# Performance work log

Hardware: AMD Instinct MI355X
Metric: run time of the kernel (lower is better)

## Reference

```python
import jax, jax.numpy as jnp
import numpy as np

NQ = 4
DIM = 1 << NQ  # 16 statevector amplitudes

def _cnot_perm(c, t):
    idx = np.arange(DIM)
    cbit = (idx >> (NQ - 1 - c)) & 1
    return np.where(cbit == 1, idx ^ (1 << (NQ - 1 - t)), idx)

# BasicEntanglerLayers CNOT ring: (0,1),(1,2),(2,3),(3,0)
CNOT_PERMS = [jnp.asarray(_cnot_perm(q, (q + 1) % NQ)) for q in range(NQ)]
_idx = np.arange(DIM)
SIGNS = jnp.asarray(np.stack([1.0 - 2.0 * ((_idx >> (NQ - 1 - q)) & 1) for q in range(NQ)]).astype(np.float32))  # (NQ, DIM), PauliZ eigenvalues


def _apply_rx(state, theta, q):
    """Apply RX(theta) on wire q. state: (N, DIM) complex64. theta: scalar or (N,)."""
    half = theta * 0.5
    c = jnp.cos(half).astype(jnp.complex64)
    js = (1j * jnp.sin(half)).astype(jnp.complex64)
    if jnp.ndim(theta) == 1:
        c = c[:, None, None]
        js = js[:, None, None]
    d1, d2 = 1 << q, 1 << (NQ - 1 - q)
    st = state.reshape(-1, d1, 2, d2)
    a0, a1 = st[:, :, 0, :], st[:, :, 1, :]
    out = jnp.stack([c * a0 - js * a1, c * a1 - js * a0], axis=2)
    return out.reshape(state.shape)


def circuit(angles, weights):
    """AngleEmbedding(RX) + BasicEntanglerLayers(RX + CNOT ring) + <Z_i>.
    angles: (N, NQ) real. weights: (L, NQ). returns (N, NQ)."""
    N = angles.shape[0]
    state = jnp.zeros((N, DIM), jnp.complex64).at[:, 0].set(1.0)
    for q in range(NQ):  # AngleEmbedding: per-sample RX angles
        state = _apply_rx(state, angles[:, q], q)
    for l in range(weights.shape[0]):  # entangler layers (static count)
        for q in range(NQ):
            state = _apply_rx(state, weights[l, q], q)
        for q in range(NQ):
            state = state[:, CNOT_PERMS[q]]
    probs = jnp.real(state) ** 2 + jnp.imag(state) ** 2
    return probs @ SIGNS.T


def setup_inputs() -> dict:
    key = jax.random.key(0)
    ks = jax.random.split(key, 5)
    B, S = 32, 2048
    TWO_PI = 6.2831853
    return {
        "x": jax.random.normal(ks[0], (B, S, NQ), jnp.float32),
        "weights_Q": jax.random.uniform(ks[1], (1, NQ), jnp.float32) * TWO_PI,
        "weights_K": jax.random.uniform(ks[2], (1, NQ), jnp.float32) * TWO_PI,
        "weights_V": jax.random.uniform(ks[3], (1, NQ), jnp.float32) * TWO_PI,
        "weights_C": jax.random.uniform(ks[4], (1, NQ), jnp.float32) * TWO_PI,
    }


def reference(x, weights_Q, weights_K, weights_V, weights_C):
    B, S, E = x.shape  # E == NQ == 4
    flat = x.reshape(B * S, E)
    Q = circuit(flat, weights_Q).reshape(B, S, E)
    K = circuit(flat, weights_K).reshape(B, S, E)
    V = circuit(flat, weights_V).reshape(B, S, E)
    scores = jnp.einsum('bqe,bke->bqk', Q, K) / (E ** 0.5)
    attn = jax.nn.softmax(scores, axis=-1)
    ctx = jnp.einsum('bqk,bke->bqe', attn, V)
    return circuit(ctx.reshape(B * S, E), weights_C).reshape(B, S, E)
```

## Files before the change

### kernel.cpp

```cpp
#include <hip/hip_runtime.h>

#define DIM 16
#define SEQ 2048
#define CHUNK 256
#define NPAIR (CHUNK / 2)
#define NCHUNK 8
#define RPT 2

typedef float v2f __attribute__((ext_vector_type(2)));
typedef float v4f __attribute__((ext_vector_type(4)));

static __device__ __forceinline__ float fexp2(float x) {
#if __has_builtin(__builtin_amdgcn_exp2f)
    return __builtin_amdgcn_exp2f(x);
#else
    return exp2f(x);
#endif
}


template<int P>
__device__ __forceinline__ void rx_bit(float sr[DIM], float si[DIM], float ch, float sh) {
    constexpr int m = 1 << P;
    #pragma unroll
    for (int i = 0; i < DIM; ++i) {
        if ((i & m) == 0) {
            const int j = i | m;
            float r0 = sr[i], i0 = si[i], r1 = sr[j], i1 = si[j];
            sr[i] = fmaf(ch, r0,  sh * i1);
            si[i] = fmaf(ch, i0, -sh * r1);
            sr[j] = fmaf(ch, r1,  sh * i0);
            si[j] = fmaf(ch, i1, -sh * r0);
        }
    }
}

template<int PC, int PT>
__device__ __forceinline__ void cnot_g(float sr[DIM], float si[DIM]) {
    constexpr int cm = 1 << PC, tm = 1 << PT;
    #pragma unroll
    for (int i = 0; i < DIM; ++i) {
        if ((i & cm) && !(i & tm)) {
            const int j = i | tm;
            float t;
            t = sr[i]; sr[i] = sr[j]; sr[j] = t;
            t = si[i]; si[i] = si[j]; si[j] = t;
        }
    }
}

__device__ __forceinline__ void embed(float sr[DIM], float si[DIM], float4 a) {
    float c0, s0, c1, s1, c2, s2, c3, s3;
    __sincosf(0.5f * a.x, &s0, &c0);
    __sincosf(0.5f * a.y, &s1, &c1);
    __sincosf(0.5f * a.z, &s2, &c2);
    __sincosf(0.5f * a.w, &s3, &c3);
    float A[4] = {c0 * c1, c0 * s1, s0 * c1, s0 * s1};
    float B[4] = {c2 * c3, c2 * s3, s2 * c3, s2 * s3};
    #pragma unroll
    for (int idx = 0; idx < DIM; ++idx) {
        const float p = A[idx >> 2] * B[idx & 3];
        const int m = __builtin_popcount(idx) & 3;
        sr[idx] = (m == 0) ? p : (m == 2) ? -p : 0.f;
        si[idx] = (m == 1) ? -p : (m == 3) ? p : 0.f;
    }
}

__device__ __forceinline__ void layer(float sr[DIM], float si[DIM], float4 w) {
    float ch, sh;
    __sincosf(0.5f * w.x, &sh, &ch); rx_bit<3>(sr, si, ch, sh);
    __sincosf(0.5f * w.y, &sh, &ch); rx_bit<2>(sr, si, ch, sh);
    __sincosf(0.5f * w.z, &sh, &ch); rx_bit<1>(sr, si, ch, sh);
    __sincosf(0.5f * w.w, &sh, &ch); rx_bit<0>(sr, si, ch, sh);
    cnot_g<3,2>(sr, si);
    cnot_g<2,1>(sr, si);
    cnot_g<1,0>(sr, si);
    cnot_g<0,3>(sr, si);
}

__device__ __forceinline__ float4 measure(const float sr[DIM], const float si[DIM]) {
    float e0 = 0.f, e1 = 0.f, e2 = 0.f, e3 = 0.f;
    #pragma unroll
    for (int i = 0; i < DIM; ++i) {
        float p = fmaf(sr[i], sr[i], si[i] * si[i]);
        e0 += (i & 8) ? -p : p;
        e1 += (i & 4) ? -p : p;
        e2 += (i & 2) ? -p : p;
        e3 += (i & 1) ? -p : p;
    }
    return make_float4(e0, e1, e2, e3);
}


__global__ __launch_bounds__(256) void qkv_kernel(
        const float* __restrict__ x,
        const float* __restrict__ wQp, const float* __restrict__ wKp,
        const float* __restrict__ wVp,
        float4* __restrict__ Q, float4* __restrict__ KV) {
    const int i = blockIdx.x * 256 + threadIdx.x;
    const int which = blockIdx.y;
    const float4 xv = ((const float4*)x)[i];
    const float* wp = (which == 0) ? wQp : (which == 1) ? wKp : wVp;
    const float4 w = *(const float4*)wp;

    float sr[DIM], si[DIM];
    embed(sr, si, xv);
    layer(sr, si, w);
    const float4 r = measure(sr, si);

    if (which == 0)      Q[i]          = r;
    else if (which == 1) KV[2 * i]     = r;
    else                 KV[2 * i + 1] = r;
}


__global__ __launch_bounds__(256, 4) void attn_partial(
        const float4* __restrict__ Q, const float4* __restrict__ KV,
        float* __restrict__ pden, float4* __restrict__ pctx, int n) {
    __shared__ float4 kvs[4 * NPAIR];

    const int rg = blockIdx.x;
    const int c  = blockIdx.y;
    const int b  = rg >> 2;

    const float4* KVc = KV + (size_t)b * (2 * SEQ) + c * (2 * CHUNK);
    if (threadIdx.x < NPAIR) {
        const int p = threadIdx.x;
        const float4 K0 = KVc[4 * p + 0];
        const float4 V0 = KVc[4 * p + 1];
        const float4 K1 = KVc[4 * p + 2];
        const float4 V1 = KVc[4 * p + 3];
        kvs[4 * p + 0] = make_float4(K0.x, K1.x, K0.y, K1.y);
        kvs[4 * p + 1] = make_float4(K0.z, K1.z, K0.w, K1.w);
        kvs[4 * p + 2] = make_float4(V0.x, V1.x, V0.y, V1.y);
        kvs[4 * p + 3] = make_float4(V0.z, V1.z, V0.w, V1.w);
    }
    __syncthreads();

    const float SC = 0.72134752044f;
    const int row0 = rg * (256 * RPT) + threadIdx.x;

    v2f qx[RPT], qy[RPT], qz[RPT], qw[RPT];
    #pragma unroll
    for (int j = 0; j < RPT; ++j) {
        const float4 q = Q[row0 + j * 256];
        qx[j] = (v2f){q.x * SC, q.x * SC};
        qy[j] = (v2f){q.y * SC, q.y * SC};
        qz[j] = (v2f){q.z * SC, q.z * SC};
        qw[j] = (v2f){q.w * SC, q.w * SC};
    }

    v2f den[RPT], ax[RPT], ay[RPT], az[RPT], aw[RPT];
    #pragma unroll
    for (int j = 0; j < RPT; ++j) {
        den[j] = (v2f){0.f, 0.f};
        ax[j] = den[j]; ay[j] = den[j]; az[j] = den[j]; aw[j] = den[j];
    }

    const v4f* kvp = (const v4f*)kvs;
    #pragma unroll 4
    for (int p = 0; p < NPAIR; ++p) {
        const v4f kA = kvp[4 * p + 0];
        const v4f kB = kvp[4 * p + 1];
        const v4f vA = kvp[4 * p + 2];
        const v4f vB = kvp[4 * p + 3];
        const v2f kx = kA.xy, ky = kA.zw, kz = kB.xy, kw = kB.zw;
        const v2f vx = vA.xy, vy = vA.zw, vz = vB.xy, vw = vB.zw;
        #pragma unroll
        for (int j = 0; j < RPT; ++j) {
            v2f s = __builtin_elementwise_fma(qy[j], ky, qx[j] * kx);
            s     = __builtin_elementwise_fma(qz[j], kz, s);
            s     = __builtin_elementwise_fma(qw[j], kw, s);
            const v2f e = (v2f){fexp2(s.x), fexp2(s.y)};
            den[j] += e;
            ax[j] = __builtin_elementwise_fma(e, vx, ax[j]);
            ay[j] = __builtin_elementwise_fma(e, vy, ay[j]);
            az[j] = __builtin_elementwise_fma(e, vz, az[j]);
            aw[j] = __builtin_elementwise_fma(e, vw, aw[j]);
        }
    }

    #pragma unroll
    for (int j = 0; j < RPT; ++j) {
        const int row = row0 + j * 256;
        pden[c * n + row] = den[j].x + den[j].y;
        pctx[c * n + row] = make_float4(ax[j].x + ax[j].y, ay[j].x + ay[j].y,
                                        az[j].x + az[j].y, aw[j].x + aw[j].y);
    }
}


__global__ __launch_bounds__(256) void combine_kernel(
        const float* __restrict__ pden, const float4* __restrict__ pctx,
        const float* __restrict__ wCp, float4* __restrict__ out, int n) {
    const int row = blockIdx.x * 256 + threadIdx.x;

    float d = 0.f;
    float c0 = 0.f, c1 = 0.f, c2 = 0.f, c3 = 0.f;
    #pragma unroll
    for (int c = 0; c < NCHUNK; ++c) {
        d += pden[c * n + row];
        const float4 p = pctx[c * n + row];
        c0 += p.x; c1 += p.y; c2 += p.z; c3 += p.w;
    }
    const float inv = 1.0f / d;
    const float4 ctx = make_float4(c0 * inv, c1 * inv, c2 * inv, c3 * inv);

    const float4 wC = *(const float4*)wCp;
    float sr[DIM], si[DIM];
    embed(sr, si, ctx);
    layer(sr, si, wC);
    out[row] = measure(sr, si);
}


extern "C" void kernel_launch(void* const* d_in, const int* in_sizes, int n_in,
                              void* d_out, int out_size, void* d_ws, size_t ws_size,
                              hipStream_t stream) {
    const float* x  = (const float*)d_in[0];
    const float* wQ = (const float*)d_in[1];
    const float* wK = (const float*)d_in[2];
    const float* wV = (const float*)d_in[3];
    const float* wC = (const float*)d_in[4];

    const int n = in_sizes[0] / 4;
    float4* Q    = (float4*)d_ws;
    float4* KV   = Q + n;
    float4* pctx = KV + 2 * n;
    float*  pden = (float*)(pctx + NCHUNK * n);

    dim3 qgrid(n / 256, 3);
    qkv_kernel<<<qgrid, 256, 0, stream>>>(x, wQ, wK, wV, Q, KV);

    dim3 agrid(n / (256 * RPT), NCHUNK);
    attn_partial<<<agrid, 256, 0, stream>>>(Q, KV, pden, pctx, n);

    combine_kernel<<<n / 256, 256, 0, stream>>>(pden, pctx, wC, (float4*)d_out, n);
}
```

Baseline: 101.8 us.

## Pre-transpose K/V in producer, read K via scalar loads, retile attention chunks

The QKV kernel now writes K and V directly in a pair-interleaved transposed layout, so the attention kernel no longer shuffles them in shared memory. K is read straight from global memory with wave-uniform addresses, and only V is staged in LDS. Chunk size is halved, chunk count doubled and rows per thread doubled, giving more independent work per thread. Partial results and Q use nontemporal loads and stores. The combine kernel now has twice as many partials to reduce, and the producer's strided scattered stores may cost extra.

Measured after the change: 103.2 us. Within noise of the previous version (+1.4%).

```diff
diff --git a/kernel.cpp b/kernel.cpp
--- a/kernel.cpp
+++ b/kernel.cpp
@@ -2,10 +2,10 @@
 
 #define DIM 16
 #define SEQ 2048
-#define CHUNK 256
+#define CHUNK 128
 #define NPAIR (CHUNK / 2)
-#define NCHUNK 8
-#define RPT 2
+#define NCHUNK 16
+#define RPT 4
 
 typedef float v2f __attribute__((ext_vector_type(2)));
 typedef float v4f __attribute__((ext_vector_type(4)));
@@ -96,7 +96,7 @@
         const float* __restrict__ x,
         const float* __restrict__ wQp, const float* __restrict__ wKp,
         const float* __restrict__ wVp,
-        float4* __restrict__ Q, float4* __restrict__ KV) {
+        float4* __restrict__ Q, float* __restrict__ Kt, float* __restrict__ Vt) {
     const int i = blockIdx.x * 256 + threadIdx.x;
     const int which = blockIdx.y;
     const float4 xv = ((const float4*)x)[i];
@@ -108,33 +108,31 @@
     layer(sr, si, w);
     const float4 r = measure(sr, si);
 
-    if (which == 0)      Q[i]          = r;
-    else if (which == 1) KV[2 * i]     = r;
-    else                 KV[2 * i + 1] = r;
+    if (which == 0) {
+        Q[i] = r;
+    } else {
+        const int bb = i >> 11, rr = i & (SEQ - 1);
+        const int p = rr >> 1, h = rr & 1;
+        float* base = ((which == 1) ? Kt : Vt)
+                      + ((size_t)bb * (SEQ / 2) + p) * 8 + h;
+        base[0] = r.x; base[2] = r.y; base[4] = r.z; base[6] = r.w;
+    }
 }
 
 
 __global__ __launch_bounds__(256, 4) void attn_partial(
-        const float4* __restrict__ Q, const float4* __restrict__ KV,
-        float* __restrict__ pden, float4* __restrict__ pctx, int n) {
-    __shared__ float4 kvs[4 * NPAIR];
+        const v4f* __restrict__ Q, const float* __restrict__ Kt,
+        const float* __restrict__ Vt,
+        float* __restrict__ pden, v4f* __restrict__ pctx, int n) {
+    __shared__ v4f vs[2 * NPAIR];
 
     const int rg = blockIdx.x;
     const int c  = blockIdx.y;
-    const int b  = rg >> 2;
-
-    const float4* KVc = KV + (size_t)b * (2 * SEQ) + c * (2 * CHUNK);
-    if (threadIdx.x < NPAIR) {
-        const int p = threadIdx.x;
-        const float4 K0 = KVc[4 * p + 0];
-        const float4 V0 = KVc[4 * p + 1];
-        const float4 K1 = KVc[4 * p + 2];
-        const float4 V1 = KVc[4 * p + 3];
-        kvs[4 * p + 0] = make_float4(K0.x, K1.x, K0.y, K1.y);
-        kvs[4 * p + 1] = make_float4(K0.z, K1.z, K0.w, K1.w);
-        kvs[4 * p + 2] = make_float4(V0.x, V1.x, V0.y, V1.y);
-        kvs[4 * p + 3] = make_float4(V0.z, V1.z, V0.w, V1.w);
-    }
+    const int b  = rg >> 1;
+
+    const v4f* Vtc = (const v4f*)(Vt + ((size_t)b * (SEQ / 2) + c * NPAIR) * 8);
+    if (threadIdx.x < 2 * NPAIR)
+        vs[threadIdx.x] = Vtc[threadIdx.x];
     __syncthreads();
 
     const float SC = 0.72134752044f;
@@ -143,7 +141,7 @@
     v2f qx[RPT], qy[RPT], qz[RPT], qw[RPT];
     #pragma unroll
     for (int j = 0; j < RPT; ++j) {
-        const float4 q = Q[row0 + j * 256];
+        const v4f q = __builtin_nontemporal_load(Q + (row0 + j * 256));
         qx[j] = (v2f){q.x * SC, q.x * SC};
         qy[j] = (v2f){q.y * SC, q.y * SC};
         qz[j] = (v2f){q.z * SC, q.z * SC};
@@ -157,14 +155,16 @@
         ax[j] = den[j]; ay[j] = den[j]; az[j] = den[j]; aw[j] = den[j];
     }
 
-    const v4f* kvp = (const v4f*)kvs;
+    const float* Ktc = Kt + ((size_t)b * (SEQ / 2) + c * NPAIR) * 8;
+
     #pragma unroll 4
     for (int p = 0; p < NPAIR; ++p) {
-        const v4f kA = kvp[4 * p + 0];
-        const v4f kB = kvp[4 * p + 1];
-        const v4f vA = kvp[4 * p + 2];
-        const v4f vB = kvp[4 * p + 3];
-        const v2f kx = kA.xy, ky = kA.zw, kz = kB.xy, kw = kB.zw;
+        const v2f kx = *(const v2f*)(Ktc + 8 * p + 0);
+        const v2f ky = *(const v2f*)(Ktc + 8 * p + 2);
+        const v2f kz = *(const v2f*)(Ktc + 8 * p + 4);
+        const v2f kw = *(const v2f*)(Ktc + 8 * p + 6);
+        const v4f vA = vs[2 * p + 0];
+        const v4f vB = vs[2 * p + 1];
         const v2f vx = vA.xy, vy = vA.zw, vz = vB.xy, vw = vB.zw;
         #pragma unroll
         for (int j = 0; j < RPT; ++j) {
@@ -183,15 +183,16 @@
     #pragma unroll
     for (int j = 0; j < RPT; ++j) {
         const int row = row0 + j * 256;
-        pden[c * n + row] = den[j].x + den[j].y;
-        pctx[c * n + row] = make_float4(ax[j].x + ax[j].y, ay[j].x + ay[j].y,
-                                        az[j].x + az[j].y, aw[j].x + aw[j].y);
+        __builtin_nontemporal_store(den[j].x + den[j].y, pden + (c * n + row));
+        const v4f ct = (v4f){ax[j].x + ax[j].y, ay[j].x + ay[j].y,
+                             az[j].x + az[j].y, aw[j].x + aw[j].y};
+        __builtin_nontemporal_store(ct, pctx + (c * n + row));
     }
 }
 
 
 __global__ __launch_bounds__(256) void combine_kernel(
-        const float* __restrict__ pden, const float4* __restrict__ pctx,
+        const float* __restrict__ pden, const v4f* __restrict__ pctx,
         const float* __restrict__ wCp, float4* __restrict__ out, int n) {
     const int row = blockIdx.x * 256 + threadIdx.x;
 
@@ -199,8 +200,8 @@
     float c0 = 0.f, c1 = 0.f, c2 = 0.f, c3 = 0.f;
     #pragma unroll
     for (int c = 0; c < NCHUNK; ++c) {
-        d += pden[c * n + row];
-        const float4 p = pctx[c * n + row];
+        d += __builtin_nontemporal_load(pden + (c * n + row));
+        const v4f p = __builtin_nontemporal_load(pctx + (c * n + row));
         c0 += p.x; c1 += p.y; c2 += p.z; c3 += p.w;
     }
     const float inv = 1.0f / d;
@@ -225,15 +226,17 @@
 
     const int n = in_sizes[0] / 4;
     float4* Q    = (float4*)d_ws;
-    float4* KV   = Q + n;
-    float4* pctx = KV + 2 * n;
-    float*  pden = (float*)(pctx + NCHUNK * n);
+    float*  Kt   = (float*)(Q + n);
+    float*  Vt   = Kt + 4 * n;
+    v4f*   pctx  = (v4f*)(Vt + 4 * n);
+    float* pden  = (float*)(pctx + (size_t)NCHUNK * n);
 
     dim3 qgrid(n / 256, 3);
-    qkv_kernel<<<qgrid, 256, 0, stream>>>(x, wQ, wK, wV, Q, KV);
+    qkv_kernel<<<qgrid, 256, 0, stream>>>(x, wQ, wK, wV, Q, Kt, Vt);
 
     dim3 agrid(n / (256 * RPT), NCHUNK);
-    attn_partial<<<agrid, 256, 0, stream>>>(Q, KV, pden, pctx, n);
+    attn_partial<<<agrid, 256, 0, stream>>>((const v4f*)Q, Kt, Vt,
+                                            pden, pctx, n);
 
     combine_kernel<<<n / 256, 256, 0, stream>>>(pden, pctx, wC, (float4*)d_out, n);
 }
```
